# Optimization experiments

Measured on AMD Instinct MI355X. Metric: run time of the kernel, lower is better.

## Reference

```python
import jax, jax.numpy as jnp
import numpy as np

NEG_SLOPE = 0.01  # torch leaky_relu default


def _conv1x3(x, w, b):
    # x: (B, C_in, N, T), w: (C_out, C_in, 1, 3) -> (B, C_out, N, T-2)
    y = jax.lax.conv_general_dilated(x, w, window_strides=(1, 1), padding='VALID',
                                     dimension_numbers=('NCHW', 'OIHW', 'NCHW'))
    return y + b[None, :, None, None]


def _timeblock(X, cw1, cb1, cw2, cb2, cw3, cb3):
    # X: (B, N, T, C_in) -> (B, N, T-2, C_out)
    x = jnp.transpose(X, (0, 3, 1, 2))
    temp = _conv1x3(x, cw1, cb1) + jax.nn.sigmoid(_conv1x3(x, cw2, cb2))
    out = jax.nn.relu(temp + _conv1x3(x, cw3, cb3))
    return jnp.transpose(out, (0, 2, 3, 1))


def setup_inputs() -> dict:
    key = jax.random.key(0)
    ks = jax.random.split(key, 10)
    B, N, T, Cin, Cout = 8, 2048, 64, 16, 4
    att_dim = T - 2  # 62
    D = att_dim * Cout  # 248 per node; fc in_features = 2*D = 496
    X = jax.random.normal(ks[0], (B, N, T, Cin), dtype=jnp.float32)
    # sparse-ish binary adjacency
    A = jax.random.randint(ks[1], (N, N), 0, 2).astype(jnp.float32)
    s = 0.05
    cw1 = jax.random.normal(ks[2], (Cout, Cin, 1, 3), dtype=jnp.float32) * s
    cb1 = jax.random.normal(ks[3], (Cout,), dtype=jnp.float32) * s
    cw2 = jax.random.normal(ks[4], (Cout, Cin, 1, 3), dtype=jnp.float32) * s
    cb2 = jax.random.normal(ks[5], (Cout,), dtype=jnp.float32) * s
    cw3 = jax.random.normal(ks[6], (Cout, Cin, 1, 3), dtype=jnp.float32) * s
    cb3 = jax.random.normal(ks[7], (Cout,), dtype=jnp.float32) * s
    fcw = jax.random.normal(ks[8], (2 * D,), dtype=jnp.float32) * s
    fcb = jax.random.normal(ks[9], (), dtype=jnp.float32) * s
    return {"X": X, "A": A, "cw1": cw1, "cb1": cb1, "cw2": cw2, "cb2": cb2,
            "cw3": cw3, "cb3": cb3, "fcw": fcw, "fcb": fcb}


def reference(X, A, cw1, cb1, cw2, cb2, cw3, cb3, fcw, fcb):
    t = _timeblock(X, cw1, cb1, cw2, cb2, cw3, cb3)  # (B, N, T-2, 4)
    B, N, To, C = t.shape
    D = To * C
    tf = t.reshape(B, N, D)
    wi, wj = fcw[:D], fcw[D:]
    si = tf @ wi  # (B, N) contribution of source node i
    sj = tf @ wj  # (B, N) contribution of target node j
    scores = jax.nn.leaky_relu(si[:, :, None] + sj[:, None, :] + fcb, NEG_SLOPE)
    mask = (A != 0.0)[None]  # entries for zero edges stay 0 before softmax
    att = jnp.where(mask, scores, 0.0)
    soft = jax.nn.softmax(att, axis=2)
    return soft * A[None]
```

## Files before the change

### kernel.cpp

```cpp
#include <hip/hip_runtime.h>
#include <cfloat>

#define N_NODES 2048
#define BN_TOTAL 16384

typedef float vf4 __attribute__((ext_vector_type(4)));

__global__ __launch_bounds__(256) void k_sisj(
    const float* __restrict__ X,
    const float* __restrict__ cw1, const float* __restrict__ cb1,
    const float* __restrict__ cw2, const float* __restrict__ cb2,
    const float* __restrict__ cw3, const float* __restrict__ cb3,
    const float* __restrict__ fcw,
    float* __restrict__ si, float* __restrict__ sj)
{
    __shared__ float tile[2][1024];
    __shared__ float red[4][2][2];

    const int tid  = threadIdx.x;
    const int wid  = tid >> 6;
    const int lane = tid & 63;
    const int bn0  = blockIdx.x * 2;

    {
        const vf4 v0 = *(const vf4*)(X + (size_t)bn0 * 1024 + tid * 4);
        const vf4 v1 = *(const vf4*)(X + (size_t)(bn0 + 1) * 1024 + tid * 4);
        *(vf4*)&tile[0][tid * 4] = v0;
        *(vf4*)&tile[1][tid * 4] = v1;
    }
    __syncthreads();

    const int c_u = __builtin_amdgcn_readfirstlane(wid);
    const float* __restrict__ w1 = cw1 + c_u * 48;
    const float* __restrict__ w2 = cw2 + c_u * 48;
    const float* __restrict__ w3 = cw3 + c_u * 48;
    const float b1 = cb1[c_u], b2 = cb2[c_u], b3 = cb3[c_u];

    const int to = lane;
    float t0 = 0.f, t1 = 0.f;

    if (to < 62) {
        vf4 xr0[3][4], xr1[3][4];
        #pragma unroll
        for (int dt = 0; dt < 3; ++dt)
            #pragma unroll
            for (int q = 0; q < 4; ++q) {
                xr0[dt][q] = *(const vf4*)&tile[0][(to + dt) * 16 + q * 4];
                xr1[dt][q] = *(const vf4*)&tile[1][(to + dt) * 16 + q * 4];
            }
        const float* xf0 = (const float*)xr0;
        const float* xf1 = (const float*)xr1;

        float acc0[3] = {b1, b2, b3};
        float acc1[3] = {b1, b2, b3};
        const float* __restrict__ wp[3] = {w1, w2, w3};
        #pragma unroll
        for (int k = 0; k < 3; ++k) {
            float wk[48];
            #pragma unroll
            for (int q = 0; q < 12; ++q)
                *(vf4*)&wk[q * 4] = *(const vf4*)(wp[k] + q * 4);
            float a0 = acc0[k], a1 = acc1[k];
            #pragma unroll
            for (int ci = 0; ci < 16; ++ci)
                #pragma unroll
                for (int dt = 0; dt < 3; ++dt) {
                    const float w = wk[ci * 3 + dt];
                    a0 = fmaf(xf0[dt * 16 + ci], w, a0);
                    a1 = fmaf(xf1[dt * 16 + ci], w, a1);
                }
            acc0[k] = a0; acc1[k] = a1;
        }
        const float s0 = 1.f / (1.f + __expf(-acc0[1]));
        const float s1 = 1.f / (1.f + __expf(-acc1[1]));
        const float v0 = acc0[0] + s0 + acc0[2];
        const float v1 = acc1[0] + s1 + acc1[2];
        t0 = v0 > 0.f ? v0 : 0.f;
        t1 = v1 > 0.f ? v1 : 0.f;
    }

    float pi0 = 0.f, pj0 = 0.f, pi1 = 0.f, pj1 = 0.f;
    if (to < 62) {
        const float wi = fcw[to * 4 + c_u];
        const float wj = fcw[248 + to * 4 + c_u];
        pi0 = t0 * wi; pj0 = t0 * wj;
        pi1 = t1 * wi; pj1 = t1 * wj;
    }
    #pragma unroll
    for (int off = 32; off > 0; off >>= 1) {
        pi0 += __shfl_xor(pi0, off);
        pj0 += __shfl_xor(pj0, off);
        pi1 += __shfl_xor(pi1, off);
        pj1 += __shfl_xor(pj1, off);
    }
    if (lane == 0) {
        red[wid][0][0] = pi0; red[wid][0][1] = pj0;
        red[wid][1][0] = pi1; red[wid][1][1] = pj1;
    }
    __syncthreads();
    if (tid < 4) {
        const int n = tid >> 1, cmp = tid & 1;
        const float s = red[0][n][cmp] + red[1][n][cmp] + red[2][n][cmp] + red[3][n][cmp];
        float* __restrict__ dst = cmp ? sj : si;
        dst[bn0 + n] = s;
    }
}

__global__ __launch_bounds__(256) void k_att(
    const float* __restrict__ A,
    const float* __restrict__ si, const float* __restrict__ sj,
    const float* __restrict__ fcb,
    float* __restrict__ out)
{
    __shared__ float reds[4];

    const int blk   = blockIdx.x;
    const int xcd   = blk & 7;
    const int local = blk >> 3;
    const int i     = (xcd << 8) | (local & 255);
    const int b     = local >> 8;
    const int row   = b * N_NODES + i;
    const int tid   = threadIdx.x;

    const float cbase = si[row] + fcb[0];
    const float* __restrict__ sjb = sj + b * N_NODES;
    const float* __restrict__ Ar  = A + (size_t)i * N_NODES;

    float avv[8], att[8];
    float sum = 0.f;
    #pragma unroll
    for (int u = 0; u < 2; ++u) {
        const int j4 = tid + u * 256;
        const vf4 a4 = ((const vf4*)Ar)[j4];
        const vf4 s4 = ((const vf4*)sjb)[j4];
        #pragma unroll
        for (int q = 0; q < 4; ++q) {
            float s = cbase + s4[q];
            s = (s >= 0.f) ? s : 0.01f * s;
            const float at_ = (a4[q] != 0.f) ? s : 0.f;
            const float e = __expf(at_);
            avv[u * 4 + q] = a4[q];
            att[u * 4 + q] = e;
            sum += e;
        }
    }

    #pragma unroll
    for (int off = 32; off > 0; off >>= 1) sum += __shfl_xor(sum, off);
    if ((tid & 63) == 0) reds[tid >> 6] = sum;
    __syncthreads();
    sum = reds[0] + reds[1] + reds[2] + reds[3];

    const float inv = 1.f / sum;
    float* __restrict__ orow = out + (size_t)row * N_NODES;
    #pragma unroll
    for (int u = 0; u < 2; ++u) {
        const int j4 = tid + u * 256;
        vf4 o;
        o[0] = avv[u * 4 + 0] * (att[u * 4 + 0] * inv);
        o[1] = avv[u * 4 + 1] * (att[u * 4 + 1] * inv);
        o[2] = avv[u * 4 + 2] * (att[u * 4 + 2] * inv);
        o[3] = avv[u * 4 + 3] * (att[u * 4 + 3] * inv);
        __builtin_nontemporal_store(o, (vf4*)orow + j4);
    }
}

extern "C" void kernel_launch(void* const* d_in, const int* in_sizes, int n_in,
                              void* d_out, int out_size, void* d_ws, size_t ws_size,
                              hipStream_t stream)
{
    const float* X   = (const float*)d_in[0];
    const float* A   = (const float*)d_in[1];
    const float* cw1 = (const float*)d_in[2];
    const float* cb1 = (const float*)d_in[3];
    const float* cw2 = (const float*)d_in[4];
    const float* cb2 = (const float*)d_in[5];
    const float* cw3 = (const float*)d_in[6];
    const float* cb3 = (const float*)d_in[7];
    const float* fcw = (const float*)d_in[8];
    const float* fcb = (const float*)d_in[9];
    float* out = (float*)d_out;

    float* si = (float*)d_ws;
    float* sj = si + BN_TOTAL;

    hipLaunchKernelGGL(k_sisj, dim3(BN_TOTAL / 2), dim3(256), 0, stream,
                       X, cw1, cb1, cw2, cb2, cw3, cb3, fcw, si, sj);
    hipLaunchKernelGGL(k_att, dim3(BN_TOTAL), dim3(256), 0, stream,
                       A, si, sj, fcb, out);
}
```

Measured before the change: 223.8 us.

## Reuse adjacency rows across batches and compute all channels per wave

The attention kernel now launches one block per node row i and processes all 8 batches inside it. Each A row is loaded once with nontemporal loads instead of once per batch, and the exponentials are recomputed in the store pass rather than held in registers. The conv kernel maps one (b,n) pair to each wave, computing all 4 output channels per lane, which removes the cross-wave shared-memory reduction and the second barrier. The trade-offs are much higher register pressure (8x2 vf4 of sj per thread), fewer blocks in the attention kernel, double the exp work, and dropping the XCD-aware block mapping.

```diff
diff --git a/kernel.cpp b/kernel.cpp
--- a/kernel.cpp
+++ b/kernel.cpp
@@ -1,5 +1,4 @@
 #include <hip/hip_runtime.h>
-#include <cfloat>
 
 #define N_NODES 2048
 #define BN_TOTAL 16384
@@ -14,95 +13,75 @@
     const float* __restrict__ fcw,
     float* __restrict__ si, float* __restrict__ sj)
 {
-    __shared__ float tile[2][1024];
-    __shared__ float red[4][2][2];
-
+    __shared__ float Xs[4096];
     const int tid  = threadIdx.x;
     const int wid  = tid >> 6;
     const int lane = tid & 63;
-    const int bn0  = blockIdx.x * 2;
+    const int bn0  = blockIdx.x * 4;
 
-    {
-        const vf4 v0 = *(const vf4*)(X + (size_t)bn0 * 1024 + tid * 4);
-        const vf4 v1 = *(const vf4*)(X + (size_t)(bn0 + 1) * 1024 + tid * 4);
-        *(vf4*)&tile[0][tid * 4] = v0;
-        *(vf4*)&tile[1][tid * 4] = v1;
+    #pragma unroll
+    for (int q = 0; q < 4; ++q) {
+        const int idx = q * 256 + tid;
+        *(vf4*)&Xs[idx * 4] = *(const vf4*)(X + (size_t)bn0 * 1024 + (size_t)idx * 4);
     }
     __syncthreads();
 
-    const int c_u = __builtin_amdgcn_readfirstlane(wid);
-    const float* __restrict__ w1 = cw1 + c_u * 48;
-    const float* __restrict__ w2 = cw2 + c_u * 48;
-    const float* __restrict__ w3 = cw3 + c_u * 48;
-    const float b1 = cb1[c_u], b2 = cb2[c_u], b3 = cb3[c_u];
+    const int to = lane;
+    const float* __restrict__ xb = &Xs[wid * 1024];
 
-    const int to = lane;
-    float t0 = 0.f, t1 = 0.f;
-
+    float pi = 0.f, pj = 0.f;
     if (to < 62) {
-        vf4 xr0[3][4], xr1[3][4];
+        vf4 xr[12];
         #pragma unroll
         for (int dt = 0; dt < 3; ++dt)
             #pragma unroll
-            for (int q = 0; q < 4; ++q) {
-                xr0[dt][q] = *(const vf4*)&tile[0][(to + dt) * 16 + q * 4];
-                xr1[dt][q] = *(const vf4*)&tile[1][(to + dt) * 16 + q * 4];
+            for (int q = 0; q < 4; ++q)
+                xr[dt * 4 + q] = *(const vf4*)&xb[(to + dt) * 16 + q * 4];
+        const float* xf = (const float*)xr;
+
+        const vf4 b1 = *(const vf4*)cb1;
+        const vf4 b2 = *(const vf4*)cb2;
+        const vf4 b3 = *(const vf4*)cb3;
+
+        float acc[12];
+        #pragma unroll
+        for (int c = 0; c < 4; ++c) { acc[c] = b1[c]; acc[4 + c] = b2[c]; acc[8 + c] = b3[c]; }
+
+        const float* __restrict__ cw[3] = {cw1, cw2, cw3};
+        #pragma unroll
+        for (int k = 0; k < 3; ++k)
+            #pragma unroll
+            for (int c = 0; c < 4; ++c) {
+                const float* __restrict__ w = cw[k] + c * 48;
+                float a = acc[k * 4 + c];
+                #pragma unroll
+                for (int ci = 0; ci < 16; ++ci)
+                    #pragma unroll
+                    for (int dt = 0; dt < 3; ++dt)
+                        a = fmaf(xf[dt * 16 + ci], w[ci * 3 + dt], a);
+                acc[k * 4 + c] = a;
             }
-        const float* xf0 = (const float*)xr0;
-        const float* xf1 = (const float*)xr1;
 
-        float acc0[3] = {b1, b2, b3};
-        float acc1[3] = {b1, b2, b3};
-        const float* __restrict__ wp[3] = {w1, w2, w3};
+        const vf4 wiv = *(const vf4*)(fcw + to * 4);
+        const vf4 wjv = *(const vf4*)(fcw + 248 + to * 4);
         #pragma unroll
-        for (int k = 0; k < 3; ++k) {
-            float wk[48];
-            #pragma unroll
-            for (int q = 0; q < 12; ++q)
-                *(vf4*)&wk[q * 4] = *(const vf4*)(wp[k] + q * 4);
-            float a0 = acc0[k], a1 = acc1[k];
-            #pragma unroll
-            for (int ci = 0; ci < 16; ++ci)
-                #pragma unroll
-                for (int dt = 0; dt < 3; ++dt) {
-                    const float w = wk[ci * 3 + dt];
-                    a0 = fmaf(xf0[dt * 16 + ci], w, a0);
-                    a1 = fmaf(xf1[dt * 16 + ci], w, a1);
-                }
-            acc0[k] = a0; acc1[k] = a1;
+        for (int c = 0; c < 4; ++c) {
+            const float sig = 1.f / (1.f + __expf(-acc[4 + c]));
+            const float tv  = acc[c] + sig + acc[8 + c];
+            const float t   = tv > 0.f ? tv : 0.f;
+            pi = fmaf(t, wiv[c], pi);
+            pj = fmaf(t, wjv[c], pj);
         }
-        const float s0 = 1.f / (1.f + __expf(-acc0[1]));
-        const float s1 = 1.f / (1.f + __expf(-acc1[1]));
-        const float v0 = acc0[0] + s0 + acc0[2];
-        const float v1 = acc1[0] + s1 + acc1[2];
-        t0 = v0 > 0.f ? v0 : 0.f;
-        t1 = v1 > 0.f ? v1 : 0.f;
     }
 
-    float pi0 = 0.f, pj0 = 0.f, pi1 = 0.f, pj1 = 0.f;
-    if (to < 62) {
-        const float wi = fcw[to * 4 + c_u];
-        const float wj = fcw[248 + to * 4 + c_u];
-        pi0 = t0 * wi; pj0 = t0 * wj;
-        pi1 = t1 * wi; pj1 = t1 * wj;
-    }
     #pragma unroll
     for (int off = 32; off > 0; off >>= 1) {
-        pi0 += __shfl_xor(pi0, off);
-        pj0 += __shfl_xor(pj0, off);
-        pi1 += __shfl_xor(pi1, off);
-        pj1 += __shfl_xor(pj1, off);
+        pi += __shfl_xor(pi, off);
+        pj += __shfl_xor(pj, off);
     }
     if (lane == 0) {
-        red[wid][0][0] = pi0; red[wid][0][1] = pj0;
-        red[wid][1][0] = pi1; red[wid][1][1] = pj1;
-    }
-    __syncthreads();
-    if (tid < 4) {
-        const int n = tid >> 1, cmp = tid & 1;
-        const float s = red[0][n][cmp] + red[1][n][cmp] + red[2][n][cmp] + red[3][n][cmp];
-        float* __restrict__ dst = cmp ? sj : si;
-        dst[bn0 + n] = s;
+        si[bn0 + wid] = pi;
+        sj[bn0 + wid] = pj;
     }
 }
 
@@ -112,56 +91,64 @@
     const float* __restrict__ fcb,
     float* __restrict__ out)
 {
-    __shared__ float reds[4];
+    __shared__ float red[8][4];
 
-    const int blk   = blockIdx.x;
-    const int xcd   = blk & 7;
-    const int local = blk >> 3;
-    const int i     = (xcd << 8) | (local & 255);
-    const int b     = local >> 8;
-    const int row   = b * N_NODES + i;
-    const int tid   = threadIdx.x;
+    const int i    = blockIdx.x;
+    const int tid  = threadIdx.x;
+    const int wid  = tid >> 6;
+    const int lane = tid & 63;
 
-    const float cbase = si[row] + fcb[0];
-    const float* __restrict__ sjb = sj + b * N_NODES;
-    const float* __restrict__ Ar  = A + (size_t)i * N_NODES;
+    const vf4* __restrict__ Ar = (const vf4*)(A + (size_t)i * N_NODES);
+    vf4 a4[2];
+    a4[0] = __builtin_nontemporal_load(Ar + tid);
+    a4[1] = __builtin_nontemporal_load(Ar + tid + 256);
 
-    float avv[8], att[8];
-    float sum = 0.f;
+    vf4 sjv[8][2];
     #pragma unroll
-    for (int u = 0; u < 2; ++u) {
-        const int j4 = tid + u * 256;
-        const vf4 a4 = ((const vf4*)Ar)[j4];
-        const vf4 s4 = ((const vf4*)sjb)[j4];
-        #pragma unroll
-        for (int q = 0; q < 4; ++q) {
-            float s = cbase + s4[q];
-            s = (s >= 0.f) ? s : 0.01f * s;
-            const float at_ = (a4[q] != 0.f) ? s : 0.f;
-            const float e = __expf(at_);
-            avv[u * 4 + q] = a4[q];
-            att[u * 4 + q] = e;
-            sum += e;
-        }
+    for (int b = 0; b < 8; ++b) {
+        const vf4* __restrict__ sb = (const vf4*)(sj + b * N_NODES);
+        sjv[b][0] = sb[tid];
+        sjv[b][1] = sb[tid + 256];
     }
+    const float fcb0 = fcb[0];
+    float cb[8];
+    #pragma unroll
+    for (int b = 0; b < 8; ++b) cb[b] = si[b * N_NODES + i] + fcb0;
 
     #pragma unroll
-    for (int off = 32; off > 0; off >>= 1) sum += __shfl_xor(sum, off);
-    if ((tid & 63) == 0) reds[tid >> 6] = sum;
+    for (int b = 0; b < 8; ++b) {
+        float s = 0.f;
+        #pragma unroll
+        for (int u = 0; u < 2; ++u)
+            #pragma unroll
+            for (int q = 0; q < 4; ++q) {
+                float sc = cb[b] + sjv[b][u][q];
+                sc = (sc >= 0.f) ? sc : 0.01f * sc;
+                const float at = (a4[u][q] != 0.f) ? sc : 0.f;
+                s += __expf(at);
+            }
+        #pragma unroll
+        for (int off = 32; off > 0; off >>= 1) s += __shfl_xor(s, off);
+        if (lane == 0) red[b][wid] = s;
+    }
     __syncthreads();
-    sum = reds[0] + reds[1] + reds[2] + reds[3];
 
-    const float inv = 1.f / sum;
-    float* __restrict__ orow = out + (size_t)row * N_NODES;
     #pragma unroll
-    for (int u = 0; u < 2; ++u) {
-        const int j4 = tid + u * 256;
-        vf4 o;
-        o[0] = avv[u * 4 + 0] * (att[u * 4 + 0] * inv);
-        o[1] = avv[u * 4 + 1] * (att[u * 4 + 1] * inv);
-        o[2] = avv[u * 4 + 2] * (att[u * 4 + 2] * inv);
-        o[3] = avv[u * 4 + 3] * (att[u * 4 + 3] * inv);
-        __builtin_nontemporal_store(o, (vf4*)orow + j4);
+    for (int b = 0; b < 8; ++b) {
+        const float inv = 1.f / (red[b][0] + red[b][1] + red[b][2] + red[b][3]);
+        vf4* __restrict__ orow = (vf4*)(out + ((size_t)b * N_NODES + i) * N_NODES);
+        #pragma unroll
+        for (int u = 0; u < 2; ++u) {
+            vf4 o;
+            #pragma unroll
+            for (int q = 0; q < 4; ++q) {
+                float sc = cb[b] + sjv[b][u][q];
+                sc = (sc >= 0.f) ? sc : 0.01f * sc;
+                const float at = (a4[u][q] != 0.f) ? sc : 0.f;
+                o[q] = a4[u][q] * (__expf(at) * inv);
+            }
+            __builtin_nontemporal_store(o, orow + tid + u * 256);
+        }
     }
 }
 
@@ -184,8 +171,8 @@
     float* si = (float*)d_ws;
     float* sj = si + BN_TOTAL;
 
-    hipLaunchKernelGGL(k_sisj, dim3(BN_TOTAL / 2), dim3(256), 0, stream,
+    hipLaunchKernelGGL(k_sisj, dim3(BN_TOTAL / 4), dim3(256), 0, stream,
                        X, cw1, cb1, cw2, cb2, cw3, cb3, fcw, si, sj);
-    hipLaunchKernelGGL(k_att, dim3(BN_TOTAL), dim3(256), 0, stream,
+    hipLaunchKernelGGL(k_att, dim3(N_NODES), dim3(256), 0, stream,
                        A, si, sj, fcb, out);
 }
```

New measurement: 228.3 us. 1.02x slower.
